# Optimization experiments

Hardware: AMD Instinct MI355X
Metric: run time of the kernel (lower is better)

## Reference

```python
import jax, jax.numpy as jnp
import numpy as np

D = 512
H = 8
HD = D // H
EPS = 1e-8


def setup_inputs() -> dict:
    key = jax.random.key(0)
    ks = jax.random.split(key, 16)
    B, S = 4, 2048
    s = lambda n: 1.0 / np.sqrt(n)
    inp = {
        "gene_emb": jax.random.normal(ks[0], (B, S, D), jnp.float32),
        "expr_emb": jax.random.normal(ks[1], (B, S, D), jnp.float32),
        "M": jax.random.uniform(ks[2], (B, S, S), jnp.float32),
        # weights stored (in, out) so y = x @ W + b
        "W_fused": jax.random.normal(ks[3], (2 * D, D), jnp.float32) * s(2 * D),
        "b_fused": jnp.zeros((D,), jnp.float32),
        "W_Q": jax.random.normal(ks[4], (D, D), jnp.float32) * s(D),
        "b_Q": jnp.zeros((D,), jnp.float32),
        "W_K": jax.random.normal(ks[5], (D, D), jnp.float32) * s(D),
        "b_K": jnp.zeros((D,), jnp.float32),
        "W_V": jax.random.normal(ks[6], (D, D), jnp.float32) * s(D),
        "b_V": jnp.zeros((D,), jnp.float32),
        "W_O": jax.random.normal(ks[7], (D, D), jnp.float32) * s(D),
        "b_O": jnp.zeros((D,), jnp.float32),
    }
    return inp


def reference(gene_emb, expr_emb, M, W_fused, b_fused, W_Q, b_Q, W_K, b_K, W_V, b_V, W_O, b_O):
    B, S, _ = gene_emb.shape
    scale = HD ** (-0.5)
    fused = jnp.concatenate([gene_emb, expr_emb], axis=-1) @ W_fused + b_fused
    # (B,S,D) -> (B,H,S,HD)
    split = lambda x: x.reshape(B, S, H, HD).transpose(0, 2, 1, 3)
    Q = split(fused @ W_Q + b_Q)
    K = split(fused @ W_K + b_K)
    V = split(expr_emb @ W_V + b_V)
    scores = jnp.einsum("bhqd,bhkd->bhqk", Q, K) * scale
    Mg = M[:, None, :, :]  # broadcast over heads
    scores = scores * Mg
    attn = jax.nn.softmax(scores, axis=-1)
    A_sparse = attn * Mg
    norm = jnp.sum(jnp.abs(A_sparse), axis=-1, keepdims=True) + EPS
    A_bar = A_sparse / norm
    out = jnp.einsum("bhqk,bhkd->bhqd", A_bar, V)
    out = out.transpose(0, 2, 1, 3).reshape(B, S, D)
    return out @ W_O + b_O
```

## Files before the change

### kernel.cpp

```cpp
#include <hip/hip_runtime.h>

typedef unsigned short u16;
typedef __attribute__((ext_vector_type(8))) short bf16x8_t;
typedef __attribute__((ext_vector_type(4))) float f32x4_t;

__device__ __forceinline__ u16 f2bf(float x){
  union { float f; unsigned u; } v; v.f = x;
  unsigned r = v.u + 0x7FFFu + ((v.u >> 16) & 1u);
  return (u16)(r >> 16);
}
__device__ __forceinline__ float bf2f(u16 h){
  union { unsigned u; float f; } v; v.u = ((unsigned)h) << 16;
  return v.f;
}
__device__ __forceinline__ u16 hi16(float x){
  union { float f; unsigned u; } v; v.f = x;
  return (u16)(v.u >> 16);
}

__device__ __forceinline__ void gl2lds16(const u16* g, u16* l){
  __builtin_amdgcn_global_load_lds((const __attribute__((address_space(1))) void*)g,
                                   (__attribute__((address_space(3))) void*)l, 16, 0, 0);
}

__global__ __launch_bounds__(256) void split_concat_kernel(
    const float* __restrict__ gene, const float* __restrict__ expr,
    u16* __restrict__ Xh, u16* __restrict__ Xl)
{
  size_t e = ((size_t)blockIdx.x * 256 + threadIdx.x) * 4;
  int row = (int)(e >> 10);
  int col = (int)(e & 1023);
  const float* src = (col < 512) ? (gene + (size_t)row * 512 + col)
                                 : (expr + (size_t)row * 512 + (col - 512));
  float4 v = *(const float4*)src;
  float a[4] = {v.x, v.y, v.z, v.w};
  u16 hs[4], ls[4];
#pragma unroll
  for (int i = 0; i < 4; i++){
    hs[i] = f2bf(a[i]);
    ls[i] = f2bf(a[i] - bf2f(hs[i]));
  }
  *(uint2*)(Xh + e) = make_uint2(hs[0] | ((unsigned)hs[1] << 16), hs[2] | ((unsigned)hs[3] << 16));
  *(uint2*)(Xl + e) = make_uint2(ls[0] | ((unsigned)ls[1] << 16), ls[2] | ((unsigned)ls[3] << 16));
}

__global__ __launch_bounds__(256) void transpose_all_kernel(
    const float* __restrict__ Wf, const float* __restrict__ Wq,
    const float* __restrict__ Wk, const float* __restrict__ Wv,
    const float* __restrict__ Wo,
    u16* __restrict__ Wfth, u16* __restrict__ Wftl,
    u16* __restrict__ Wqth, u16* __restrict__ Wkth,
    u16* __restrict__ Wvth, u16* __restrict__ Woth)
{
  __shared__ float t[64][65];
  int id = blockIdx.x;
  const float* W; u16* Th; u16* Tl; int K, kx, ny;
  if (id < 128){ W = Wf; Th = Wfth; Tl = Wftl; K = 1024; kx = id >> 3; ny = id & 7; }
  else {
    int tt = id - 128; int wi = tt >> 6; tt &= 63; kx = tt >> 3; ny = tt & 7; K = 512;
    W  = (wi == 0) ? Wq  : (wi == 1) ? Wk  : (wi == 2) ? Wv  : Wo;
    Th = (wi == 0) ? Wqth: (wi == 1) ? Wkth: (wi == 2) ? Wvth: Woth;
    Tl = nullptr;
  }
  int k0 = kx * 64, n0 = ny * 64;
  int tid = threadIdx.x;
  int r = tid >> 4;
  int c4 = (tid & 15) * 4;
#pragma unroll
  for (int p = 0; p < 4; p++){
    int k = p * 16 + r;
    float4 v = *(const float4*)(W + (size_t)(k0 + k) * 512 + n0 + c4);
    t[c4 + 0][k] = v.x; t[c4 + 1][k] = v.y; t[c4 + 2][k] = v.z; t[c4 + 3][k] = v.w;
  }
  __syncthreads();
#pragma unroll
  for (int p = 0; p < 4; p++){
    int n = p * 16 + r;
    u16 hs[4], ls[4];
#pragma unroll
    for (int i = 0; i < 4; i++){
      float x = t[n][c4 + i];
      hs[i] = f2bf(x);
      ls[i] = f2bf(x - bf2f(hs[i]));
    }
    size_t o = (size_t)(n0 + n) * K + k0 + c4;
    *(uint2*)(Th + o) = make_uint2(hs[0] | ((unsigned)hs[1] << 16), hs[2] | ((unsigned)hs[3] << 16));
    if (Tl)
      *(uint2*)(Tl + o) = make_uint2(ls[0] | ((unsigned)ls[1] << 16), ls[2] | ((unsigned)ls[3] << 16));
  }
}

template<int SPLITS, int MODE, int DUAL>
__global__ __launch_bounds__(256, 2) void gemm_kernel(
    const u16* __restrict__ Ah, const u16* __restrict__ Al, int lda,
    const u16* __restrict__ Bh0, const u16* __restrict__ Bl0,
    const u16* __restrict__ Bh1, int K,
    const float* __restrict__ bias0, const float* __restrict__ bias1,
    void* __restrict__ out0, void* __restrict__ out1, void* __restrict__ outsec,
    float sc0, float sc1)
{
  __shared__ __align__(16) u16 sAh[128 * 32];
  __shared__ __align__(16) u16 sAl[SPLITS >= 2 ? 128 * 32 : 8];
  __shared__ __align__(16) u16 sBh[64 * 32];
  __shared__ __align__(16) u16 sBl[SPLITS == 3 ? 64 * 32 : 8];
  int tid = threadIdx.x;
  int lane = tid & 63, w = tid >> 6, quad = lane >> 4, l15 = lane & 15;
  int wm = w & 1, wn = w >> 1;
  int m0 = blockIdx.x * 128;
  int side = DUAL ? (int)(blockIdx.y >> 3) : 0;
  int n0 = (DUAL ? (int)(blockIdx.y & 7) : (int)blockIdx.y) * 64;
  const u16* Bh = (DUAL && side) ? Bh1 : Bh0;
  const float* bias = (DUAL && side) ? bias1 : bias0;
  void* o0 = (DUAL && side) ? outsec : out0;
  float sc = (DUAL && side) ? sc1 : sc0;

  f32x4_t acc[4][2];
#pragma unroll
  for (int i = 0; i < 4; i++)
#pragma unroll
    for (int j = 0; j < 2; j++)
#pragma unroll
      for (int r = 0; r < 4; r++) acc[i][j][r] = 0.f;

  int lrow = lane >> 2;
  int swzS = ((lane >> 2) & 3) ^ ((lane >> 4) & 3);
  int gkq  = ((lane & 3) ^ swzS) * 8;
  const u16* pAh0 = Ah + (size_t)(m0 + w * 32 + lrow) * lda + gkq;
  const u16* pAh1 = Ah + (size_t)(m0 + w * 32 + 16 + lrow) * lda + gkq;
  const u16* pAl0 = (SPLITS >= 2) ? Al + (size_t)(m0 + w * 32 + lrow) * lda + gkq : nullptr;
  const u16* pAl1 = (SPLITS >= 2) ? Al + (size_t)(m0 + w * 32 + 16 + lrow) * lda + gkq : nullptr;
  const u16* pBh0 = Bh + (size_t)(n0 + w * 16 + lrow) * K + gkq;
  const u16* pBl0 = (SPLITS == 3) ? Bl0 + (size_t)(n0 + w * 16 + lrow) * K + gkq : nullptr;
  u16* dAh = sAh + w * 1024;
  u16* dAl = sAl + w * 1024;
  u16* dBh = sBh + w * 512;
  u16* dBl = sBl + w * 512;

  int pq = (quad ^ ((l15 & 3) ^ ((l15 >> 2) & 3))) * 8;

  for (int k0 = 0; k0 < K; k0 += 32){
    __syncthreads();
    gl2lds16(pAh0 + k0, dAh);
    gl2lds16(pAh1 + k0, dAh + 512);
    if constexpr (SPLITS >= 2){
      gl2lds16(pAl0 + k0, dAl);
      gl2lds16(pAl1 + k0, dAl + 512);
    }
    gl2lds16(pBh0 + k0, dBh);
    if constexpr (SPLITS == 3)
      gl2lds16(pBl0 + k0, dBl);
    __syncthreads();

    bf16x8_t aH[4], aL[4], bH[2], bL[2];
#pragma unroll
    for (int mi = 0; mi < 4; mi++){
      int ad = (wm * 64 + mi * 16 + l15) * 32 + pq;
      aH[mi] = *(const bf16x8_t*)&sAh[ad];
      if constexpr (SPLITS >= 2) aL[mi] = *(const bf16x8_t*)&sAl[ad];
    }
#pragma unroll
    for (int ni = 0; ni < 2; ni++){
      int bd = (wn * 32 + ni * 16 + l15) * 32 + pq;
      bH[ni] = *(const bf16x8_t*)&sBh[bd];
      if constexpr (SPLITS == 3) bL[ni] = *(const bf16x8_t*)&sBl[bd];
    }
#pragma unroll
    for (int mi = 0; mi < 4; mi++)
#pragma unroll
      for (int ni = 0; ni < 2; ni++){
        acc[mi][ni] = __builtin_amdgcn_mfma_f32_16x16x32_bf16(aH[mi], bH[ni], acc[mi][ni], 0, 0, 0);
        if constexpr (SPLITS == 3)
          acc[mi][ni] = __builtin_amdgcn_mfma_f32_16x16x32_bf16(aH[mi], bL[ni], acc[mi][ni], 0, 0, 0);
        if constexpr (SPLITS >= 2)
          acc[mi][ni] = __builtin_amdgcn_mfma_f32_16x16x32_bf16(aL[mi], bH[ni], acc[mi][ni], 0, 0, 0);
      }
  }

#pragma unroll
  for (int mi = 0; mi < 4; mi++)
#pragma unroll
    for (int ni = 0; ni < 2; ni++){
      int gn = n0 + wn * 32 + ni * 16 + l15;
      float bs = bias[gn];
      int gm0 = m0 + wm * 64 + mi * 16 + quad * 4;
#pragma unroll
      for (int r = 0; r < 4; r++){
        float v = acc[mi][ni][r] + bs;
        int gm = gm0 + r;
        if constexpr (MODE == 0){
          u16 hb = f2bf(v);
          ((u16*)o0)[(size_t)gm * 512 + gn] = hb;
          ((u16*)out1)[(size_t)gm * 512 + gn] = f2bf(v - bf2f(hb));
        } else if constexpr (MODE == 1){
          ((u16*)o0)[(size_t)gm * 512 + gn] = f2bf(v * sc);
        } else if constexpr (MODE == 2){
          int bb = gm >> 11, s = gm & 2047;
          int hh = gn >> 6, d = gn & 63;
          ((u16*)o0)[((size_t)((bb * 8 + hh) * 64 + d) << 11) + s] = f2bf(v);
        } else {
          ((float*)o0)[(size_t)gm * 512 + gn] = v;
        }
      }
    }
}

__global__ __launch_bounds__(256, 4) void flash_kernel(
    const u16* __restrict__ Qh, const u16* __restrict__ Kh,
    const u16* __restrict__ Vt, const float* __restrict__ Mm,
    u16* __restrict__ Oh)
{
  __shared__ __align__(16) u16 sKh[64 * 64], sVt[64 * 64];
  __shared__ __align__(16) u16 sP[64 * 72];
  int tid = threadIdx.x, lane = tid & 63, w = tid >> 6, quad = lane >> 4, l15 = lane & 15;
  int bh = blockIdx.y, b = bh >> 3, h = bh & 7;
  int q0 = blockIdx.x * 64;

  int qrow = q0 + w * 16 + l15;
  const u16* qp = Qh + ((size_t)(b * 2048 + qrow)) * 512 + h * 64 + quad * 8;
  bf16x8_t qH[2];
  qH[0] = *(const bf16x8_t*)qp;  qH[1] = *(const bf16x8_t*)(qp + 32);

  float lp[4] = {0.f, 0.f, 0.f, 0.f};
  f32x4_t Oacc[4];
#pragma unroll
  for (int ni = 0; ni < 4; ni++)
#pragma unroll
    for (int r = 0; r < 4; r++) Oacc[ni][r] = 0.f;

  int srow = lane >> 3;
  int gc = ((lane & 7) ^ ((lane >> 3) & 7)) * 8;
  const u16* gKh0 = Kh + ((size_t)(b * 2048 + w * 16 + srow)) * 512 + h * 64 + gc;
  const u16* gVt0 = Vt + ((size_t)(bh * 64 + w * 16 + srow)) * 2048 + gc;
  u16* dKh = sKh + w * 1024;
  u16* dVt = sVt + w * 1024;
  const float* Mbase = Mm + (size_t)b * 2048 * 2048 + (size_t)(q0 + w * 16) * 2048;

  float Mc[4][4];
#pragma unroll
  for (int ni = 0; ni < 4; ni++)
#pragma unroll
    for (int r = 0; r < 4; r++)
      Mc[ni][r] = Mbase[(size_t)(quad * 4 + r) * 2048 + ni * 16 + l15];

  int sw7 = l15 & 7;
  for (int k0 = 0; k0 < 2048; k0 += 64){
    __syncthreads();
    gl2lds16(gKh0 + (size_t)k0 * 512,       dKh);
    gl2lds16(gKh0 + (size_t)(k0 + 8) * 512, dKh + 512);
    gl2lds16(gVt0 + k0,                     dVt);
    gl2lds16(gVt0 + 8 * 2048 + k0,          dVt + 512);
    __syncthreads();

    float Mn[4][4];
    bool hasNext = (k0 + 64) < 2048;
    if (hasNext){
#pragma unroll
      for (int ni = 0; ni < 4; ni++)
#pragma unroll
        for (int r = 0; r < 4; r++)
          Mn[ni][r] = Mbase[(size_t)(quad * 4 + r) * 2048 + (k0 + 64) + ni * 16 + l15];
    }

    f32x4_t Sacc[4];
#pragma unroll
    for (int ni = 0; ni < 4; ni++)
#pragma unroll
      for (int r = 0; r < 4; r++) Sacc[ni][r] = 0.f;
#pragma unroll
    for (int ni = 0; ni < 4; ni++){
      int kb = (ni * 16 + l15) * 64;
#pragma unroll
      for (int ds = 0; ds < 2; ds++){
        int p = ((ds * 4 + quad) ^ sw7) * 8;
        bf16x8_t kH = *(const bf16x8_t*)&sKh[kb + p];
        Sacc[ni] = __builtin_amdgcn_mfma_f32_16x16x32_bf16(qH[ds], kH, Sacc[ni], 0, 0, 0);
      }
    }

#pragma unroll
    for (int ni = 0; ni < 4; ni++)
#pragma unroll
      for (int r = 0; r < 4; r++){
        float m = Mc[ni][r];
        float p = m * __builtin_amdgcn_exp2f(Sacc[ni][r] * m);
        lp[r] += p;
        sP[(w * 16 + quad * 4 + r) * 72 + ni * 16 + l15] = hi16(p);
      }

#pragma unroll
    for (int ds = 0; ds < 2; ds++){
      bf16x8_t pf = *(const bf16x8_t*)&sP[(w * 16 + l15) * 72 + ds * 32 + quad * 8];
#pragma unroll
      for (int ni = 0; ni < 4; ni++){
        int p = ((ds * 4 + quad) ^ sw7) * 8;
        bf16x8_t vf = *(const bf16x8_t*)&sVt[(ni * 16 + l15) * 64 + p];
        Oacc[ni] = __builtin_amdgcn_mfma_f32_16x16x32_bf16(pf, vf, Oacc[ni], 0, 0, 0);
      }
    }

    if (hasNext){
#pragma unroll
      for (int ni = 0; ni < 4; ni++)
#pragma unroll
        for (int r = 0; r < 4; r++) Mc[ni][r] = Mn[ni][r];
    }
  }

#pragma unroll
  for (int r = 0; r < 4; r++){
#pragma unroll
    for (int off = 1; off < 16; off <<= 1)
      lp[r] += __shfl_xor(lp[r], off);
  }

#pragma unroll
  for (int r = 0; r < 4; r++){
    float inv = 1.0f / lp[r];
    int q = q0 + w * 16 + quad * 4 + r;
    size_t rb = ((size_t)(b * 2048 + q)) * 512 + h * 64;
#pragma unroll
    for (int ni = 0; ni < 4; ni++){
      float v = Oacc[ni][r] * inv;
      Oh[rb + ni * 16 + l15] = f2bf(v);
    }
  }
}

extern "C" void kernel_launch(void* const* d_in, const int* in_sizes, int n_in,
                              void* d_out, int out_size, void* d_ws, size_t ws_size,
                              hipStream_t stream)
{
  const float* gene = (const float*)d_in[0];
  const float* expr = (const float*)d_in[1];
  const float* Mm   = (const float*)d_in[2];
  const float* Wf   = (const float*)d_in[3];
  const float* bfv  = (const float*)d_in[4];
  const float* Wq   = (const float*)d_in[5];
  const float* bq   = (const float*)d_in[6];
  const float* Wk   = (const float*)d_in[7];
  const float* bk   = (const float*)d_in[8];
  const float* Wv   = (const float*)d_in[9];
  const float* bv   = (const float*)d_in[10];
  const float* Wo   = (const float*)d_in[11];
  const float* bo   = (const float*)d_in[12];
  float* out = (float*)d_out;

  char* ws = (char*)d_ws;
  size_t off = 0;
  auto alloc = [&](size_t bytes) -> void* {
    void* p = (void*)(ws + off);
    off += (bytes + 255) & ~(size_t)255;
    return p;
  };
  u16* Xh   = (u16*)alloc(8192ull * 1024 * 2);
  u16* Xl   = (u16*)alloc(8192ull * 1024 * 2);
  u16* Wfth = (u16*)alloc(512ull * 1024 * 2);
  u16* Wftl = (u16*)alloc(512ull * 1024 * 2);
  u16* Wqth = (u16*)alloc(512ull * 512 * 2);
  u16* Wkth = (u16*)alloc(512ull * 512 * 2);
  u16* Wvth = (u16*)alloc(512ull * 512 * 2);
  u16* Woth = (u16*)alloc(512ull * 512 * 2);
  u16* Fh   = (u16*)alloc(8192ull * 512 * 2);
  u16* Fl   = (u16*)alloc(8192ull * 512 * 2);
  u16* Qh   = (u16*)alloc(8192ull * 512 * 2);
  u16* Kh   = (u16*)alloc(8192ull * 512 * 2);
  u16* Vt   = (u16*)alloc(8192ull * 512 * 2);
  u16* Oh = Xh;

  const float QSC = 0.1803368801f;

  split_concat_kernel<<<8192, 256, 0, stream>>>(gene, expr, Xh, Xl);
  transpose_all_kernel<<<384, 256, 0, stream>>>(Wf, Wq, Wk, Wv, Wo,
                                                Wfth, Wftl, Wqth, Wkth, Wvth, Woth);

  gemm_kernel<3, 0, 0><<<dim3(64, 8), 256, 0, stream>>>(
      Xh, Xl, 1024, Wfth, Wftl, nullptr, 1024, bfv, nullptr, Fh, Fl, nullptr, 1.f, 1.f);
  gemm_kernel<2, 1, 1><<<dim3(64, 16), 256, 0, stream>>>(
      Fh, Fl, 512, Wqth, nullptr, Wkth, 512, bq, bk, Qh, nullptr, Kh, QSC, 1.f);
  gemm_kernel<2, 2, 0><<<dim3(64, 8), 256, 0, stream>>>(
      Xh + 512, Xl + 512, 1024, Wvth, nullptr, nullptr, 512, bv, nullptr, Vt, nullptr, nullptr, 1.f, 1.f);
  flash_kernel<<<dim3(32, 32), 256, 0, stream>>>(Qh, Kh, Vt, Mm, Oh);
  gemm_kernel<1, 3, 0><<<dim3(64, 8), 256, 0, stream>>>(
      Oh, nullptr, 512, Woth, nullptr, nullptr, 512, bo, nullptr, out, nullptr, nullptr, 1.f, 1.f);

  (void)in_sizes; (void)n_in; (void)out_size; (void)ws_size;
}
```

Before: 301.7 us.

## Merge prep kernels, fuse QKV GEMMs, deepen GEMM K-step, drop LDS in flash

The split/concat and weight-transpose kernels are merged into one launch, and the Q, K and V projections now run as one three-sided GEMM launch. The GEMM core stages 64-wide K slices per barrier instead of 32, halving the number of syncs. The flash kernel stops staging K and V through shared memory and loads the fragments straight from global memory each iteration, dropping the mask prefetch, with occupancy raised to 3 blocks. The aim is fewer launches and barriers, at the cost of uncoalesced, redundant global reads of K and V across waves and more exposed latency on the mask loads.

Result: slower. 468.7 us (+55.4%).

```diff
diff --git a/kernel.cpp b/kernel.cpp
--- a/kernel.cpp
+++ b/kernel.cpp
@@ -23,37 +23,37 @@
                                    (__attribute__((address_space(3))) void*)l, 16, 0, 0);
 }
 
-__global__ __launch_bounds__(256) void split_concat_kernel(
+__global__ __launch_bounds__(256) void prep_kernel(
     const float* __restrict__ gene, const float* __restrict__ expr,
-    u16* __restrict__ Xh, u16* __restrict__ Xl)
-{
-  size_t e = ((size_t)blockIdx.x * 256 + threadIdx.x) * 4;
-  int row = (int)(e >> 10);
-  int col = (int)(e & 1023);
-  const float* src = (col < 512) ? (gene + (size_t)row * 512 + col)
-                                 : (expr + (size_t)row * 512 + (col - 512));
-  float4 v = *(const float4*)src;
-  float a[4] = {v.x, v.y, v.z, v.w};
-  u16 hs[4], ls[4];
-#pragma unroll
-  for (int i = 0; i < 4; i++){
-    hs[i] = f2bf(a[i]);
-    ls[i] = f2bf(a[i] - bf2f(hs[i]));
-  }
-  *(uint2*)(Xh + e) = make_uint2(hs[0] | ((unsigned)hs[1] << 16), hs[2] | ((unsigned)hs[3] << 16));
-  *(uint2*)(Xl + e) = make_uint2(ls[0] | ((unsigned)ls[1] << 16), ls[2] | ((unsigned)ls[3] << 16));
-}
-
-__global__ __launch_bounds__(256) void transpose_all_kernel(
     const float* __restrict__ Wf, const float* __restrict__ Wq,
     const float* __restrict__ Wk, const float* __restrict__ Wv,
     const float* __restrict__ Wo,
+    u16* __restrict__ Xh, u16* __restrict__ Xl,
     u16* __restrict__ Wfth, u16* __restrict__ Wftl,
     u16* __restrict__ Wqth, u16* __restrict__ Wkth,
     u16* __restrict__ Wvth, u16* __restrict__ Woth)
 {
   __shared__ float t[64][65];
-  int id = blockIdx.x;
+  int tid = threadIdx.x;
+  if (blockIdx.x < 8192){
+    size_t e = ((size_t)blockIdx.x * 256 + tid) * 4;
+    int row = (int)(e >> 10);
+    int col = (int)(e & 1023);
+    const float* src = (col < 512) ? (gene + (size_t)row * 512 + col)
+                                   : (expr + (size_t)row * 512 + (col - 512));
+    float4 v = *(const float4*)src;
+    float a[4] = {v.x, v.y, v.z, v.w};
+    u16 hs[4], ls[4];
+#pragma unroll
+    for (int i = 0; i < 4; i++){
+      hs[i] = f2bf(a[i]);
+      ls[i] = f2bf(a[i] - bf2f(hs[i]));
+    }
+    *(uint2*)(Xh + e) = make_uint2(hs[0] | ((unsigned)hs[1] << 16), hs[2] | ((unsigned)hs[3] << 16));
+    *(uint2*)(Xl + e) = make_uint2(ls[0] | ((unsigned)ls[1] << 16), ls[2] | ((unsigned)ls[3] << 16));
+    return;
+  }
+  int id = blockIdx.x - 8192;
   const float* W; u16* Th; u16* Tl; int K, kx, ny;
   if (id < 128){ W = Wf; Th = Wfth; Tl = Wftl; K = 1024; kx = id >> 3; ny = id & 7; }
   else {
@@ -63,7 +63,6 @@
     Tl = nullptr;
   }
   int k0 = kx * 64, n0 = ny * 64;
-  int tid = threadIdx.x;
   int r = tid >> 4;
   int c4 = (tid & 15) * 4;
 #pragma unroll
@@ -90,92 +89,94 @@
   }
 }
 
-template<int SPLITS, int MODE, int DUAL>
-__global__ __launch_bounds__(256, 2) void gemm_kernel(
+template<int SPLITS>
+__device__ __forceinline__ void gemm_core(
     const u16* __restrict__ Ah, const u16* __restrict__ Al, int lda,
-    const u16* __restrict__ Bh0, const u16* __restrict__ Bl0,
-    const u16* __restrict__ Bh1, int K,
-    const float* __restrict__ bias0, const float* __restrict__ bias1,
-    void* __restrict__ out0, void* __restrict__ out1, void* __restrict__ outsec,
-    float sc0, float sc1)
-{
-  __shared__ __align__(16) u16 sAh[128 * 32];
-  __shared__ __align__(16) u16 sAl[SPLITS >= 2 ? 128 * 32 : 8];
-  __shared__ __align__(16) u16 sBh[64 * 32];
-  __shared__ __align__(16) u16 sBl[SPLITS == 3 ? 64 * 32 : 8];
+    const u16* __restrict__ Bh, const u16* __restrict__ Bl, int K,
+    int m0, int n0, f32x4_t (&acc)[4][2],
+    u16* sAh, u16* sAl, u16* sBh, u16* sBl)
+{
   int tid = threadIdx.x;
   int lane = tid & 63, w = tid >> 6, quad = lane >> 4, l15 = lane & 15;
   int wm = w & 1, wn = w >> 1;
-  int m0 = blockIdx.x * 128;
-  int side = DUAL ? (int)(blockIdx.y >> 3) : 0;
-  int n0 = (DUAL ? (int)(blockIdx.y & 7) : (int)blockIdx.y) * 64;
-  const u16* Bh = (DUAL && side) ? Bh1 : Bh0;
-  const float* bias = (DUAL && side) ? bias1 : bias0;
-  void* o0 = (DUAL && side) ? outsec : out0;
-  float sc = (DUAL && side) ? sc1 : sc0;
-
-  f32x4_t acc[4][2];
-#pragma unroll
-  for (int i = 0; i < 4; i++)
-#pragma unroll
-    for (int j = 0; j < 2; j++)
-#pragma unroll
-      for (int r = 0; r < 4; r++) acc[i][j][r] = 0.f;
-
   int lrow = lane >> 2;
   int swzS = ((lane >> 2) & 3) ^ ((lane >> 4) & 3);
   int gkq  = ((lane & 3) ^ swzS) * 8;
-  const u16* pAh0 = Ah + (size_t)(m0 + w * 32 + lrow) * lda + gkq;
-  const u16* pAh1 = Ah + (size_t)(m0 + w * 32 + 16 + lrow) * lda + gkq;
-  const u16* pAl0 = (SPLITS >= 2) ? Al + (size_t)(m0 + w * 32 + lrow) * lda + gkq : nullptr;
-  const u16* pAl1 = (SPLITS >= 2) ? Al + (size_t)(m0 + w * 32 + 16 + lrow) * lda + gkq : nullptr;
-  const u16* pBh0 = Bh + (size_t)(n0 + w * 16 + lrow) * K + gkq;
-  const u16* pBl0 = (SPLITS == 3) ? Bl0 + (size_t)(n0 + w * 16 + lrow) * K + gkq : nullptr;
-  u16* dAh = sAh + w * 1024;
-  u16* dAl = sAl + w * 1024;
-  u16* dBh = sBh + w * 512;
-  u16* dBl = sBl + w * 512;
-
+  const u16* pA0 = Ah + (size_t)(m0 + w * 32 + lrow) * lda + gkq;
+  const u16* pA1 = Ah + (size_t)(m0 + w * 32 + 16 + lrow) * lda + gkq;
+  const u16* pL0 = (SPLITS >= 2) ? Al + (size_t)(m0 + w * 32 + lrow) * lda + gkq : nullptr;
+  const u16* pL1 = (SPLITS >= 2) ? Al + (size_t)(m0 + w * 32 + 16 + lrow) * lda + gkq : nullptr;
+  const u16* pB0 = Bh + (size_t)(n0 + w * 16 + lrow) * K + gkq;
+  const u16* pBl = (SPLITS == 3) ? Bl + (size_t)(n0 + w * 16 + lrow) * K + gkq : nullptr;
+  u16* dA  = sAh + w * 1024;
+  u16* dAl = (SPLITS >= 2) ? sAl + w * 1024 : nullptr;
+  u16* dB  = sBh + w * 512;
+  u16* dBl = (SPLITS == 3) ? sBl + w * 512 : nullptr;
   int pq = (quad ^ ((l15 & 3) ^ ((l15 >> 2) & 3))) * 8;
 
-  for (int k0 = 0; k0 < K; k0 += 32){
+  for (int k0 = 0; k0 < K; k0 += 64){
     __syncthreads();
-    gl2lds16(pAh0 + k0, dAh);
-    gl2lds16(pAh1 + k0, dAh + 512);
-    if constexpr (SPLITS >= 2){
-      gl2lds16(pAl0 + k0, dAl);
-      gl2lds16(pAl1 + k0, dAl + 512);
-    }
-    gl2lds16(pBh0 + k0, dBh);
-    if constexpr (SPLITS == 3)
-      gl2lds16(pBl0 + k0, dBl);
+#pragma unroll
+    for (int hf = 0; hf < 2; hf++){
+      gl2lds16(pA0 + k0 + hf * 32, dA + hf * 4096);
+      gl2lds16(pA1 + k0 + hf * 32, dA + hf * 4096 + 512);
+      if constexpr (SPLITS >= 2){
+        gl2lds16(pL0 + k0 + hf * 32, dAl + hf * 4096);
+        gl2lds16(pL1 + k0 + hf * 32, dAl + hf * 4096 + 512);
+      }
+      gl2lds16(pB0 + k0 + hf * 32, dB + hf * 2048);
+      if constexpr (SPLITS == 3)
+        gl2lds16(pBl + k0 + hf * 32, dBl + hf * 2048);
+    }
     __syncthreads();
 
-    bf16x8_t aH[4], aL[4], bH[2], bL[2];
-#pragma unroll
-    for (int mi = 0; mi < 4; mi++){
-      int ad = (wm * 64 + mi * 16 + l15) * 32 + pq;
-      aH[mi] = *(const bf16x8_t*)&sAh[ad];
-      if constexpr (SPLITS >= 2) aL[mi] = *(const bf16x8_t*)&sAl[ad];
-    }
-#pragma unroll
-    for (int ni = 0; ni < 2; ni++){
-      int bd = (wn * 32 + ni * 16 + l15) * 32 + pq;
-      bH[ni] = *(const bf16x8_t*)&sBh[bd];
-      if constexpr (SPLITS == 3) bL[ni] = *(const bf16x8_t*)&sBl[bd];
-    }
-#pragma unroll
-    for (int mi = 0; mi < 4; mi++)
+#pragma unroll
+    for (int hf = 0; hf < 2; hf++){
+      bf16x8_t aH[4], aL[4], bH[2], bL[2];
+#pragma unroll
+      for (int mi = 0; mi < 4; mi++){
+        int ad = (wm * 64 + mi * 16 + l15) * 32 + pq + hf * 4096;
+        aH[mi] = *(const bf16x8_t*)&sAh[ad];
+        if constexpr (SPLITS >= 2) aL[mi] = *(const bf16x8_t*)&sAl[ad];
+      }
 #pragma unroll
       for (int ni = 0; ni < 2; ni++){
-        acc[mi][ni] = __builtin_amdgcn_mfma_f32_16x16x32_bf16(aH[mi], bH[ni], acc[mi][ni], 0, 0, 0);
-        if constexpr (SPLITS == 3)
-          acc[mi][ni] = __builtin_amdgcn_mfma_f32_16x16x32_bf16(aH[mi], bL[ni], acc[mi][ni], 0, 0, 0);
-        if constexpr (SPLITS >= 2)
-          acc[mi][ni] = __builtin_amdgcn_mfma_f32_16x16x32_bf16(aL[mi], bH[ni], acc[mi][ni], 0, 0, 0);
-      }
-  }
-
+        int bd = (wn * 32 + ni * 16 + l15) * 32 + pq + hf * 2048;
+        bH[ni] = *(const bf16x8_t*)&sBh[bd];
+        if constexpr (SPLITS == 3) bL[ni] = *(const bf16x8_t*)&sBl[bd];
+      }
+#pragma unroll
+      for (int mi = 0; mi < 4; mi++)
+#pragma unroll
+        for (int ni = 0; ni < 2; ni++){
+          acc[mi][ni] = __builtin_amdgcn_mfma_f32_16x16x32_bf16(aH[mi], bH[ni], acc[mi][ni], 0, 0, 0);
+          if constexpr (SPLITS == 3)
+            acc[mi][ni] = __builtin_amdgcn_mfma_f32_16x16x32_bf16(aH[mi], bL[ni], acc[mi][ni], 0, 0, 0);
+          if constexpr (SPLITS >= 2)
+            acc[mi][ni] = __builtin_amdgcn_mfma_f32_16x16x32_bf16(aL[mi], bH[ni], acc[mi][ni], 0, 0, 0);
+        }
+    }
+  }
+}
+
+__global__ __launch_bounds__(256, 2) void gemm_fused_kernel(
+    const u16* __restrict__ Xh, const u16* __restrict__ Xl,
+    const u16* __restrict__ Wfth, const u16* __restrict__ Wftl,
+    const float* __restrict__ bias, u16* __restrict__ Fh, u16* __restrict__ Fl)
+{
+  __shared__ __align__(16) u16 sAh[128 * 64], sAl[128 * 64], sBh[64 * 64], sBl[64 * 64];
+  int m0 = blockIdx.x * 128, n0 = blockIdx.y * 64;
+  f32x4_t acc[4][2];
+#pragma unroll
+  for (int i = 0; i < 4; i++)
+#pragma unroll
+    for (int j = 0; j < 2; j++)
+#pragma unroll
+      for (int r = 0; r < 4; r++) acc[i][j][r] = 0.f;
+  gemm_core<3>(Xh, Xl, 1024, Wfth, Wftl, 1024, m0, n0, acc, sAh, sAl, sBh, sBl);
+
+  int lane = threadIdx.x & 63, w = threadIdx.x >> 6, quad = lane >> 4, l15 = lane & 15;
+  int wm = w & 1, wn = w >> 1;
 #pragma unroll
   for (int mi = 0; mi < 4; mi++)
 #pragma unroll
@@ -186,39 +187,117 @@
 #pragma unroll
       for (int r = 0; r < 4; r++){
         float v = acc[mi][ni][r] + bs;
+        u16 hb = f2bf(v);
+        Fh[(size_t)(gm0 + r) * 512 + gn] = hb;
+        Fl[(size_t)(gm0 + r) * 512 + gn] = f2bf(v - bf2f(hb));
+      }
+    }
+}
+
+__global__ __launch_bounds__(256, 2) void gemm_qkv_kernel(
+    const u16* __restrict__ Fh, const u16* __restrict__ Fl,
+    const u16* __restrict__ Xeh, const u16* __restrict__ Xel,
+    const u16* __restrict__ Wqth, const u16* __restrict__ Wkth, const u16* __restrict__ Wvth,
+    const float* __restrict__ bq, const float* __restrict__ bk, const float* __restrict__ bv,
+    u16* __restrict__ Q, u16* __restrict__ Kout, u16* __restrict__ Vt, float qsc)
+{
+  __shared__ __align__(16) u16 sAh[128 * 64], sAl[128 * 64], sBh[64 * 64];
+  int side = blockIdx.y >> 3;
+  int m0 = blockIdx.x * 128, n0 = (blockIdx.y & 7) * 64;
+  const u16* Ah = (side == 2) ? Xeh : Fh;
+  const u16* Al = (side == 2) ? Xel : Fl;
+  int lda = (side == 2) ? 1024 : 512;
+  const u16* Bh = (side == 0) ? Wqth : (side == 1) ? Wkth : Wvth;
+  const float* bias = (side == 0) ? bq : (side == 1) ? bk : bv;
+
+  f32x4_t acc[4][2];
+#pragma unroll
+  for (int i = 0; i < 4; i++)
+#pragma unroll
+    for (int j = 0; j < 2; j++)
+#pragma unroll
+      for (int r = 0; r < 4; r++) acc[i][j][r] = 0.f;
+  gemm_core<2>(Ah, Al, lda, Bh, nullptr, 512, m0, n0, acc, sAh, sAl, sBh, nullptr);
+
+  int lane = threadIdx.x & 63, w = threadIdx.x >> 6, quad = lane >> 4, l15 = lane & 15;
+  int wm = w & 1, wn = w >> 1;
+#pragma unroll
+  for (int mi = 0; mi < 4; mi++)
+#pragma unroll
+    for (int ni = 0; ni < 2; ni++){
+      int gn = n0 + wn * 32 + ni * 16 + l15;
+      float bs = bias[gn];
+      int gm0 = m0 + wm * 64 + mi * 16 + quad * 4;
+#pragma unroll
+      for (int r = 0; r < 4; r++){
+        float v = acc[mi][ni][r] + bs;
         int gm = gm0 + r;
-        if constexpr (MODE == 0){
-          u16 hb = f2bf(v);
-          ((u16*)o0)[(size_t)gm * 512 + gn] = hb;
-          ((u16*)out1)[(size_t)gm * 512 + gn] = f2bf(v - bf2f(hb));
-        } else if constexpr (MODE == 1){
-          ((u16*)o0)[(size_t)gm * 512 + gn] = f2bf(v * sc);
-        } else if constexpr (MODE == 2){
+        if (side == 0){
+          Q[(size_t)gm * 512 + gn] = f2bf(v * qsc);
+        } else if (side == 1){
+          Kout[(size_t)gm * 512 + gn] = f2bf(v);
+        } else {
           int bb = gm >> 11, s = gm & 2047;
           int hh = gn >> 6, d = gn & 63;
-          ((u16*)o0)[((size_t)((bb * 8 + hh) * 64 + d) << 11) + s] = f2bf(v);
-        } else {
-          ((float*)o0)[(size_t)gm * 512 + gn] = v;
+          Vt[((size_t)((bb * 8 + hh) * 64 + d) << 11) + s] = f2bf(v);
         }
       }
     }
 }
 
-__global__ __launch_bounds__(256, 4) void flash_kernel(
+__global__ __launch_bounds__(256, 2) void gemm_o_kernel(
+    const u16* __restrict__ Oh, const u16* __restrict__ Woth,
+    const float* __restrict__ bias, float* __restrict__ out)
+{
+  __shared__ __align__(16) u16 sAh[128 * 64], sBh[64 * 64];
+  int m0 = blockIdx.x * 128, n0 = blockIdx.y * 64;
+  f32x4_t acc[4][2];
+#pragma unroll
+  for (int i = 0; i < 4; i++)
+#pragma unroll
+    for (int j = 0; j < 2; j++)
+#pragma unroll
+      for (int r = 0; r < 4; r++) acc[i][j][r] = 0.f;
+  gemm_core<1>(Oh, nullptr, 512, Woth, nullptr, 512, m0, n0, acc, sAh, nullptr, sBh, nullptr);
+
+  int lane = threadIdx.x & 63, w = threadIdx.x >> 6, quad = lane >> 4, l15 = lane & 15;
+  int wm = w & 1, wn = w >> 1;
+#pragma unroll
+  for (int mi = 0; mi < 4; mi++)
+#pragma unroll
+    for (int ni = 0; ni < 2; ni++){
+      int gn = n0 + wn * 32 + ni * 16 + l15;
+      float bs = bias[gn];
+      int gm0 = m0 + wm * 64 + mi * 16 + quad * 4;
+#pragma unroll
+      for (int r = 0; r < 4; r++)
+        out[(size_t)(gm0 + r) * 512 + gn] = acc[mi][ni][r] + bs;
+    }
+}
+
+__global__ __launch_bounds__(256, 3) void flash_kernel(
     const u16* __restrict__ Qh, const u16* __restrict__ Kh,
     const u16* __restrict__ Vt, const float* __restrict__ Mm,
     u16* __restrict__ Oh)
 {
-  __shared__ __align__(16) u16 sKh[64 * 64], sVt[64 * 64];
   __shared__ __align__(16) u16 sP[64 * 72];
   int tid = threadIdx.x, lane = tid & 63, w = tid >> 6, quad = lane >> 4, l15 = lane & 15;
   int bh = blockIdx.y, b = bh >> 3, h = bh & 7;
   int q0 = blockIdx.x * 64;
 
-  int qrow = q0 + w * 16 + l15;
-  const u16* qp = Qh + ((size_t)(b * 2048 + qrow)) * 512 + h * 64 + quad * 8;
-  bf16x8_t qH[2];
-  qH[0] = *(const bf16x8_t*)qp;  qH[1] = *(const bf16x8_t*)(qp + 32);
+  const u16* qp = Qh + ((size_t)(b * 2048 + q0 + w * 16 + l15)) * 512 + h * 64 + quad * 8;
+  bf16x8_t qH0 = *(const bf16x8_t*)qp;
+  bf16x8_t qH1 = *(const bf16x8_t*)(qp + 32);
+
+  const u16* pK[4]; const u16* pV[4]; const float* pM[4];
+#pragma unroll
+  for (int ni = 0; ni < 4; ni++){
+    pK[ni] = Kh + ((size_t)(b * 2048 + ni * 16 + l15)) * 512 + h * 64 + quad * 8;
+    pV[ni] = Vt + ((size_t)(bh * 64 + ni * 16 + l15)) * 2048 + quad * 8;
+  }
+#pragma unroll
+  for (int r = 0; r < 4; r++)
+    pM[r] = Mm + (size_t)b * 2048 * 2048 + (size_t)(q0 + w * 16 + quad * 4 + r) * 2048 + l15;
 
   float lp[4] = {0.f, 0.f, 0.f, 0.f};
   f32x4_t Oacc[4];
@@ -227,54 +306,36 @@
 #pragma unroll
     for (int r = 0; r < 4; r++) Oacc[ni][r] = 0.f;
 
-  int srow = lane >> 3;
-  int gc = ((lane & 7) ^ ((lane >> 3) & 7)) * 8;
-  const u16* gKh0 = Kh + ((size_t)(b * 2048 + w * 16 + srow)) * 512 + h * 64 + gc;
-  const u16* gVt0 = Vt + ((size_t)(bh * 64 + w * 16 + srow)) * 2048 + gc;
-  u16* dKh = sKh + w * 1024;
-  u16* dVt = sVt + w * 1024;
-  const float* Mbase = Mm + (size_t)b * 2048 * 2048 + (size_t)(q0 + w * 16) * 2048;
-
-  float Mc[4][4];
-#pragma unroll
-  for (int ni = 0; ni < 4; ni++)
-#pragma unroll
-    for (int r = 0; r < 4; r++)
-      Mc[ni][r] = Mbase[(size_t)(quad * 4 + r) * 2048 + ni * 16 + l15];
-
-  int sw7 = l15 & 7;
-  for (int k0 = 0; k0 < 2048; k0 += 64){
-    __syncthreads();
-    gl2lds16(gKh0 + (size_t)k0 * 512,       dKh);
-    gl2lds16(gKh0 + (size_t)(k0 + 8) * 512, dKh + 512);
-    gl2lds16(gVt0 + k0,                     dVt);
-    gl2lds16(gVt0 + 8 * 2048 + k0,          dVt + 512);
-    __syncthreads();
-
-    float Mn[4][4];
-    bool hasNext = (k0 + 64) < 2048;
-    if (hasNext){
-#pragma unroll
-      for (int ni = 0; ni < 4; ni++)
-#pragma unroll
-        for (int r = 0; r < 4; r++)
-          Mn[ni][r] = Mbase[(size_t)(quad * 4 + r) * 2048 + (k0 + 64) + ni * 16 + l15];
-    }
-
-    f32x4_t Sacc[4];
+  for (int it = 0; it < 32; ++it){
+    bf16x8_t kf[4][2];
+#pragma unroll
+    for (int ni = 0; ni < 4; ni++){
+      kf[ni][0] = *(const bf16x8_t*)(pK[ni]);
+      kf[ni][1] = *(const bf16x8_t*)(pK[ni] + 32);
+    }
+    float Mc[4][4];
 #pragma unroll
     for (int ni = 0; ni < 4; ni++)
 #pragma unroll
-      for (int r = 0; r < 4; r++) Sacc[ni][r] = 0.f;
+      for (int r = 0; r < 4; r++)
+        Mc[ni][r] = pM[r][ni * 16];
+
+    f32x4_t S[4];
+#pragma unroll
+    for (int ni = 0; ni < 4; ni++)
+#pragma unroll
+      for (int r = 0; r < 4; r++) S[ni][r] = 0.f;
 #pragma unroll
     for (int ni = 0; ni < 4; ni++){
-      int kb = (ni * 16 + l15) * 64;
-#pragma unroll
-      for (int ds = 0; ds < 2; ds++){
-        int p = ((ds * 4 + quad) ^ sw7) * 8;
-        bf16x8_t kH = *(const bf16x8_t*)&sKh[kb + p];
-        Sacc[ni] = __builtin_amdgcn_mfma_f32_16x16x32_bf16(qH[ds], kH, Sacc[ni], 0, 0, 0);
-      }
+      S[ni] = __builtin_amdgcn_mfma_f32_16x16x32_bf16(qH0, kf[ni][0], S[ni], 0, 0, 0);
+      S[ni] = __builtin_amdgcn_mfma_f32_16x16x32_bf16(qH1, kf[ni][1], S[ni], 0, 0, 0);
+    }
+
+    bf16x8_t vf[4][2];
+#pragma unroll
+    for (int ni = 0; ni < 4; ni++){
+      vf[ni][0] = *(const bf16x8_t*)(pV[ni]);
+      vf[ni][1] = *(const bf16x8_t*)(pV[ni] + 32);
     }
 
 #pragma unroll
@@ -282,7 +343,7 @@
 #pragma unroll
       for (int r = 0; r < 4; r++){
         float m = Mc[ni][r];
-        float p = m * __builtin_amdgcn_exp2f(Sacc[ni][r] * m);
+        float p = m * __builtin_amdgcn_exp2f(S[ni][r] * m);
         lp[r] += p;
         sP[(w * 16 + quad * 4 + r) * 72 + ni * 16 + l15] = hi16(p);
       }
@@ -291,19 +352,17 @@
     for (int ds = 0; ds < 2; ds++){
       bf16x8_t pf = *(const bf16x8_t*)&sP[(w * 16 + l15) * 72 + ds * 32 + quad * 8];
 #pragma unroll
-      for (int ni = 0; ni < 4; ni++){
-        int p = ((ds * 4 + quad) ^ sw7) * 8;
-        bf16x8_t vf = *(const bf16x8_t*)&sVt[(ni * 16 + l15) * 64 + p];
-        Oacc[ni] = __builtin_amdgcn_mfma_f32_16x16x32_bf16(pf, vf, Oacc[ni], 0, 0, 0);
-      }
-    }
-
-    if (hasNext){
-#pragma unroll
       for (int ni = 0; ni < 4; ni++)
-#pragma unroll
-        for (int r = 0; r < 4; r++) Mc[ni][r] = Mn[ni][r];
-    }
+        Oacc[ni] = __builtin_amdgcn_mfma_f32_16x16x32_bf16(pf, vf[ni][ds], Oacc[ni], 0, 0, 0);
+    }
+
+#pragma unroll
+    for (int ni = 0; ni < 4; ni++){
+      pK[ni] += 64 * 512;
+      pV[ni] += 64;
+    }
+#pragma unroll
+    for (int r = 0; r < 4; r++) pM[r] += 64;
   }
 
 #pragma unroll
@@ -319,10 +378,8 @@
     int q = q0 + w * 16 + quad * 4 + r;
     size_t rb = ((size_t)(b * 2048 + q)) * 512 + h * 64;
 #pragma unroll
-    for (int ni = 0; ni < 4; ni++){
-      float v = Oacc[ni][r] * inv;
-      Oh[rb + ni * 16 + l15] = f2bf(v);
-    }
+    for (int ni = 0; ni < 4; ni++)
+      Oh[rb + ni * 16 + l15] = f2bf(Oacc[ni][r] * inv);
   }
 }
 
@@ -369,19 +426,14 @@
 
   const float QSC = 0.1803368801f;
 
-  split_concat_kernel<<<8192, 256, 0, stream>>>(gene, expr, Xh, Xl);
-  transpose_all_kernel<<<384, 256, 0, stream>>>(Wf, Wq, Wk, Wv, Wo,
-                                                Wfth, Wftl, Wqth, Wkth, Wvth, Woth);
-
-  gemm_kernel<3, 0, 0><<<dim3(64, 8), 256, 0, stream>>>(
-      Xh, Xl, 1024, Wfth, Wftl, nullptr, 1024, bfv, nullptr, Fh, Fl, nullptr, 1.f, 1.f);
-  gemm_kernel<2, 1, 1><<<dim3(64, 16), 256, 0, stream>>>(
-      Fh, Fl, 512, Wqth, nullptr, Wkth, 512, bq, bk, Qh, nullptr, Kh, QSC, 1.f);
-  gemm_kernel<2, 2, 0><<<dim3(64, 8), 256, 0, stream>>>(
-      Xh + 512, Xl + 512, 1024, Wvth, nullptr, nullptr, 512, bv, nullptr, Vt, nullptr, nullptr, 1.f, 1.f);
+  prep_kernel<<<8576, 256, 0, stream>>>(gene, expr, Wf, Wq, Wk, Wv, Wo,
+                                        Xh, Xl, Wfth, Wftl, Wqth, Wkth, Wvth, Woth);
+  gemm_fused_kernel<<<dim3(64, 8), 256, 0, stream>>>(Xh, Xl, Wfth, Wftl, bfv, Fh, Fl);
+  gemm_qkv_kernel<<<dim3(64, 24), 256, 0, stream>>>(Fh, Fl, Xh + 512, Xl + 512,
+                                                    Wqth, Wkth, Wvth, bq, bk, bv,
+                                                    Qh, Kh, Vt, QSC);
   flash_kernel<<<dim3(32, 32), 256, 0, stream>>>(Qh, Kh, Vt, Mm, Oh);
-  gemm_kernel<1, 3, 0><<<dim3(64, 8), 256, 0, stream>>>(
-      Oh, nullptr, 512, Woth, nullptr, nullptr, 512, bo, nullptr, out, nullptr, nullptr, 1.f, 1.f);
+  gemm_o_kernel<<<dim3(64, 8), 256, 0, stream>>>(Oh, Woth, bo, out);
 
   (void)in_sizes; (void)n_in; (void)out_size; (void)ws_size;
 }
```
